# Optimization experiments

Hardware: AMD Instinct MI355X
Metric: run time of the kernel (lower is better)

## Reference

```python
import jax, jax.numpy as jnp
import numpy as np

SEQ, D = 4096, 1024  # vector_size == dimension == 1024


def setup_inputs() -> dict:
    key = jax.random.key(0)
    ks = jax.random.split(key, 7)
    s = 1.0 / np.sqrt(D)
    return {
        "X": jax.random.normal(ks[0], (SEQ, D), dtype=jnp.float32),
        "Wq": jax.random.normal(ks[1], (D, D), dtype=jnp.float32) * s,
        "bq": jax.random.normal(ks[2], (D,), dtype=jnp.float32) * s,
        "Wk": jax.random.normal(ks[3], (D, D), dtype=jnp.float32) * s,
        "bk": jax.random.normal(ks[4], (D,), dtype=jnp.float32) * s,
        "Wv": jax.random.normal(ks[5], (D, D), dtype=jnp.float32) * s,
        "bv": jax.random.normal(ks[6], (D,), dtype=jnp.float32) * s,
    }


def reference(X, Wq, bq, Wk, bk, Wv, bv):
    # Batched QKV projections (nn.Linear: x @ W^T + b), replacing the per-vector loop.
    Q = X @ Wq.T + bq            # [S, D]
    K = X @ Wk.T + bk            # [S, D]
    V = X @ Wv.T + bv            # [S, D]
    scale = 1.0 / jnp.sqrt(jnp.asarray(D, dtype=X.dtype))
    scores = (Q @ K.T) * scale   # [S, S]
    attn = jax.nn.softmax(scores, axis=1)
    return attn @ V              # [S, D]
```

## Files before the change

kernel.cpp:

```cpp
#include <hip/hip_runtime.h>
#include <hip/hip_bf16.h>
#include <stdint.h>


typedef __bf16 bf16_t;
typedef __bf16 bf16x4 __attribute__((ext_vector_type(4)));
typedef __bf16 bf16x8 __attribute__((ext_vector_type(8)));
typedef float f32x4 __attribute__((ext_vector_type(4)));

#define AS1 __attribute__((address_space(1)))
#define AS3 __attribute__((address_space(3)))

__device__ __forceinline__ void async_ld16(const void* g, void* l) {
  __builtin_amdgcn_global_load_lds((AS1 void*)g, (AS3 void*)l, 16, 0, 0);
}

template <int MODE>
__global__ __launch_bounds__(512, 2) void gemm8(
    const bf16_t* __restrict__ A, const bf16_t* __restrict__ B, const int ld,
    const int Klen, bf16_t* __restrict__ o0, bf16_t* __restrict__ o1,
    bf16_t* __restrict__ o2, const float* __restrict__ b0,
    const float* __restrict__ b1, const float* __restrict__ b2,
    float* __restrict__ fout, float* __restrict__ rowsum) {
  extern __shared__ bf16_t smem[];

  const int t = threadIdx.x;
  const int lane = t & 63;
  const int wave = t >> 6;
  const int wm = wave >> 2;
  const int wn = wave & 3;
  const int q = lane >> 4;
  const int l16 = lane & 15;
  const int xf = l16 & 7;

  int m0, n0, k0 = 0, zz = 0;
  const int bid = blockIdx.x;
  if constexpr (MODE == 0) {
    const int x = bid & 7, sl = bid >> 3;
    m0 = ((x >> 1) * 4 + (sl & 3)) * 256;
    n0 = ((x & 1) * 6 + (sl >> 2)) * 256;
  } else if constexpr (MODE == 1) {
    const int x = bid & 7, sl = bid >> 3;
    m0 = ((x >> 2) * 8 + (sl >> 2)) * 256;
    n0 = ((x & 3) * 4 + (sl & 3)) * 256;
  } else {
    const int x = bid & 7, sl = bid >> 3;
    zz = x >> 1;
    m0 = ((x & 1) * 8 + (sl >> 2)) * 256;
    n0 = (sl & 3) * 256;
    k0 = zz * Klen;
  }

  const int srow = t >> 3;
  const int c8s = ((t & 7) ^ (srow & 7)) * 8;
  const bf16_t* Ab = A + (size_t)(m0 + srow) * ld + k0 + c8s;
  const bf16_t* Bb = B + (size_t)(n0 + srow) * ld + k0 + c8s;
  const int tl8 = t * 8;

  const int aoff = (wm * 128 + l16) * 64;
  const int boff = (wn * 64 + l16) * 64;
  const int c0 = (q ^ xf) * 8;
  const int c1 = ((4 + q) ^ xf) * 8;

  f32x4 acc[8][4];
  const f32x4 zero4 = {0.f, 0.f, 0.f, 0.f};
#pragma unroll
  for (int i = 0; i < 8; ++i)
#pragma unroll
    for (int j = 0; j < 4; ++j) acc[i][j] = zero4;

  const int NT = Klen >> 6;
  bf16_t* buf0 = smem;
  bf16_t* buf1 = smem + 32768;

  auto STAGE = [&](int T, bf16_t* buf) {
    const size_t kk = (size_t)(T << 6);
    async_ld16(Ab + kk, buf + tl8);
    async_ld16(Ab + (size_t)64 * ld + kk, buf + 4096 + tl8);
    async_ld16(Ab + (size_t)128 * ld + kk, buf + 8192 + tl8);
    async_ld16(Ab + (size_t)192 * ld + kk, buf + 12288 + tl8);
    async_ld16(Bb + kk, buf + 16384 + tl8);
    async_ld16(Bb + (size_t)64 * ld + kk, buf + 16384 + 4096 + tl8);
    async_ld16(Bb + (size_t)128 * ld + kk, buf + 16384 + 8192 + tl8);
    async_ld16(Bb + (size_t)192 * ld + kk, buf + 16384 + 12288 + tl8);
  };

  STAGE(0, buf0);
  __syncthreads();

  for (int T = 0; T < NT; ++T) {
    bf16_t* cur = (T & 1) ? buf1 : buf0;
    bf16_t* nxt = (T & 1) ? buf0 : buf1;
    if (T + 1 < NT) STAGE(T + 1, nxt);

#pragma unroll
    for (int s = 0; s < 2; ++s) {
      const int cs = (s == 0) ? c0 : c1;
      bf16x8 fa[8], fb[4];
#pragma unroll
      for (int im = 0; im < 8; ++im)
        fa[im] = *(const bf16x8*)(cur + aoff + im * 1024 + cs);
#pragma unroll
      for (int j = 0; j < 4; ++j)
        fb[j] = *(const bf16x8*)(cur + 16384 + boff + j * 1024 + cs);
#pragma unroll
      for (int im = 0; im < 8; ++im)
#pragma unroll
        for (int j = 0; j < 4; ++j)
          acc[im][j] = __builtin_amdgcn_mfma_f32_16x16x32_bf16(
              fa[im], fb[j], acc[im][j], 0, 0, 0);
    }
    __syncthreads();
  }

  const int mW = m0 + wm * 128 + q * 4;

  if constexpr (MODE == 0) {
    const int sel = n0 >> 10;
    const int nl0 = (n0 & 1023) + wn * 64 + l16;
    if (sel < 2) {
      const float* bias = (sel == 0) ? b0 : b1;
      const float sc = (sel == 0) ? 0.03125f : 1.0f;
      bf16_t* dst = (sel == 0) ? o0 : o1;
      float bb[4];
#pragma unroll
      for (int j = 0; j < 4; ++j) bb[j] = bias[nl0 + j * 16];
#pragma unroll
      for (int im = 0; im < 8; ++im) {
        const int mr = mW + im * 16;
#pragma unroll
        for (int r = 0; r < 4; ++r)
#pragma unroll
          for (int j = 0; j < 4; ++j)
            dst[(size_t)(mr + r) * 1024 + nl0 + j * 16] =
                (bf16_t)((acc[im][j][r] + bb[j]) * sc);
      }
    } else {
      bf16_t* vs = smem;
      const int dg0 = n0 & 1023;
#pragma unroll
      for (int h = 0; h < 2; ++h) {
        if ((wn >> 1) == h) {
#pragma unroll
          for (int j = 0; j < 4; ++j) {
            const int dl = (wn & 1) * 64 + j * 16 + l16;
            const float bb = b2[dg0 + h * 128 + dl];
#pragma unroll
            for (int im = 0; im < 8; ++im) {
              bf16x4 v;
#pragma unroll
              for (int r = 0; r < 4; ++r) v[r] = (bf16_t)(acc[im][j][r] + bb);
              *(bf16x4*)(vs + dl * 264 + wm * 128 + im * 16 + q * 4) = v;
            }
          }
        }
        __syncthreads();
#pragma unroll
        for (int rr = 0; rr < 8; ++rr) {
          const int task = rr * 512 + t;
          const int row = task >> 5, ck = task & 31;
          *(bf16x8*)(o2 + (size_t)(dg0 + h * 128 + row) * 4096 + m0 + ck * 8) =
              *(const bf16x8*)(vs + row * 264 + ck * 8);
        }
        __syncthreads();
      }
    }
  } else if constexpr (MODE == 1) {
    float ps[8][4];
#pragma unroll
    for (int im = 0; im < 8; ++im)
#pragma unroll
      for (int r = 0; r < 4; ++r) ps[im][r] = 0.f;
    const int nb = n0 + wn * 64 + l16;
#pragma unroll
    for (int im = 0; im < 8; ++im) {
      const int mr = mW + im * 16;
#pragma unroll
      for (int r = 0; r < 4; ++r)
#pragma unroll
        for (int j = 0; j < 4; ++j) {
          const float e = __expf(acc[im][j][r]);
          ps[im][r] += e;
          o0[(size_t)(mr + r) * 4096 + nb + j * 16] = (bf16_t)e;
        }
    }
#pragma unroll
    for (int im = 0; im < 8; ++im)
#pragma unroll
      for (int r = 0; r < 4; ++r) {
        float v = ps[im][r];
        v += __shfl_xor(v, 1);
        v += __shfl_xor(v, 2);
        v += __shfl_xor(v, 4);
        v += __shfl_xor(v, 8);
        ps[im][r] = v;
      }
    if (l16 == 0) {
#pragma unroll
      for (int im = 0; im < 8; ++im)
#pragma unroll
        for (int r = 0; r < 4; ++r)
          atomicAdd(rowsum + mW + im * 16 + r, ps[im][r]);
    }
  } else {
    float inv[8][4];
#pragma unroll
    for (int im = 0; im < 8; ++im)
#pragma unroll
      for (int r = 0; r < 4; ++r)
        inv[im][r] = 1.0f / rowsum[mW + im * 16 + r];
    const int nb = n0 + wn * 64 + l16;
    if (zz < 3) {
      bf16_t* pp = (zz == 0) ? o0 : ((zz == 1) ? o1 : o2);
#pragma unroll
      for (int im = 0; im < 8; ++im) {
        const int mr = mW + im * 16;
#pragma unroll
        for (int r = 0; r < 4; ++r) {
          const float iv = inv[im][r];
#pragma unroll
          for (int j = 0; j < 4; ++j)
            pp[(size_t)(mr + r) * 1024 + nb + j * 16] =
                (bf16_t)(acc[im][j][r] * iv);
        }
      }
    } else {
#pragma unroll
      for (int im = 0; im < 8; ++im) {
        const int mr = mW + im * 16;
#pragma unroll
        for (int r = 0; r < 4; ++r) {
          const float iv = inv[im][r];
#pragma unroll
          for (int j = 0; j < 4; ++j)
            fout[(size_t)(mr + r) * 1024 + nb + j * 16] = acc[im][j][r] * iv;
        }
      }
    }
  }
}

__global__ __launch_bounds__(256) void cvt_all(
    const float* __restrict__ X, const float* __restrict__ Wq,
    const float* __restrict__ Wk, const float* __restrict__ Wv,
    bf16_t* __restrict__ Xb, bf16_t* __restrict__ Wb,
    float* __restrict__ rowsum) {
  int i = blockIdx.x * 256 + threadIdx.x;
  if (i >= 1835008) {
    rowsum[i - 1835008] = 0.f;
    return;
  }
  const float* src;
  bf16_t* dst;
  int off;
  if (i < 1048576) {
    src = X; dst = Xb; off = i;
  } else {
    const int w = i - 1048576;
    const int sel = w >> 18;
    off = w & 0x3FFFF;
    src = (sel == 0) ? Wq : ((sel == 1) ? Wk : Wv);
    dst = Wb + (size_t)sel * (1024 * 1024);
  }
  const float4 v = ((const float4*)src)[off];
  bf16x4 o;
  o[0] = (bf16_t)v.x; o[1] = (bf16_t)v.y; o[2] = (bf16_t)v.z; o[3] = (bf16_t)v.w;
  ((bf16x4*)dst)[off] = o;
}

__global__ __launch_bounds__(256) void reduce_out(
    const bf16_t* __restrict__ p0, const bf16_t* __restrict__ p1,
    const bf16_t* __restrict__ p2, float* __restrict__ out) {
  const int i = blockIdx.x * 256 + threadIdx.x;
  const bf16x8 a = ((const bf16x8*)p0)[i];
  const bf16x8 b = ((const bf16x8*)p1)[i];
  const bf16x8 c = ((const bf16x8*)p2)[i];
  float4 lo = ((const float4*)out)[2 * i];
  float4 hi = ((const float4*)out)[2 * i + 1];
  lo.x += (float)a[0] + (float)b[0] + (float)c[0];
  lo.y += (float)a[1] + (float)b[1] + (float)c[1];
  lo.z += (float)a[2] + (float)b[2] + (float)c[2];
  lo.w += (float)a[3] + (float)b[3] + (float)c[3];
  hi.x += (float)a[4] + (float)b[4] + (float)c[4];
  hi.y += (float)a[5] + (float)b[5] + (float)c[5];
  hi.z += (float)a[6] + (float)b[6] + (float)c[6];
  hi.w += (float)a[7] + (float)b[7] + (float)c[7];
  ((float4*)out)[2 * i] = lo;
  ((float4*)out)[2 * i + 1] = hi;
}

extern "C" void kernel_launch(void* const* d_in, const int* in_sizes, int n_in,
                              void* d_out, int out_size, void* d_ws,
                              size_t ws_size, hipStream_t stream) {
  const int S = 4096, D = 1024;
  const float* X  = (const float*)d_in[0];
  const float* Wq = (const float*)d_in[1];
  const float* bq = (const float*)d_in[2];
  const float* Wk = (const float*)d_in[3];
  const float* bk = (const float*)d_in[4];
  const float* Wv = (const float*)d_in[5];
  const float* bv = (const float*)d_in[6];
  float* out = (float*)d_out;

  bf16_t* Xb = (bf16_t*)d_ws;
  bf16_t* Wb = Xb + (size_t)S * D;
  bf16_t* Qb = Wb + (size_t)3 * D * D;
  bf16_t* Kb = Qb + (size_t)S * D;
  bf16_t* Vt = Kb + (size_t)S * D;
  bf16_t* Sc = Vt + (size_t)D * S;
  float* rowsum = (float*)(Sc + (size_t)S * S);

  static int attr_set = 0;
  if (!attr_set) {
    attr_set = 1;
    (void)hipFuncSetAttribute(reinterpret_cast<const void*>(gemm8<0>),
                              hipFuncAttributeMaxDynamicSharedMemorySize,
                              131072);
    (void)hipFuncSetAttribute(reinterpret_cast<const void*>(gemm8<1>),
                              hipFuncAttributeMaxDynamicSharedMemorySize,
                              131072);
    (void)hipFuncSetAttribute(reinterpret_cast<const void*>(gemm8<2>),
                              hipFuncAttributeMaxDynamicSharedMemorySize,
                              131072);
  }

  cvt_all<<<7184, 256, 0, stream>>>(X, Wq, Wk, Wv, Xb, Wb, rowsum);

  gemm8<0><<<192, 512, 131072, stream>>>(
      Xb, Wb, D, D, Qb, Kb, Vt, bq, bk, bv, nullptr, nullptr);
  gemm8<1><<<256, 512, 131072, stream>>>(
      Qb, Kb, D, D, Sc, nullptr, nullptr, nullptr, nullptr, nullptr, nullptr,
      rowsum);
  gemm8<2><<<256, 512, 131072, stream>>>(
      Sc, Vt, S, S / 4, Xb, Qb, Kb, nullptr, nullptr, nullptr, out, rowsum);
  reduce_out<<<S * D / 8 / 256, 256, 0, stream>>>(Xb, Qb, Kb, out);
}
```

Baseline: 205.0 us.

## Shrink GEMM tiles to 256x128 with single-buffered static LDS and higher occupancy

The three GEMM phases now use 256x128 output tiles computed by a 4x2 wave grid, with twice as many blocks. The double-buffered 128KB dynamic LDS is replaced by a single-buffered 48KB static buffer, and launch bounds ask for 4 blocks per CU. The goal is to hide memory latency through more resident blocks and a higher block count instead of software prefetch. The cost is that loads no longer overlap compute within a block. Each tile also does less MMA work per byte loaded, and the register budget becomes tighter.

Result: no change. 204.8 us, median of 2 (-0.1%).

```diff
diff --git a/kernel.cpp b/kernel.cpp
--- a/kernel.cpp
+++ b/kernel.cpp
@@ -16,19 +16,21 @@
 }
 
 template <int MODE>
-__global__ __launch_bounds__(512, 2) void gemm8(
+__global__ __launch_bounds__(512, 4) void gemm2(
     const bf16_t* __restrict__ A, const bf16_t* __restrict__ B, const int ld,
     const int Klen, bf16_t* __restrict__ o0, bf16_t* __restrict__ o1,
     bf16_t* __restrict__ o2, const float* __restrict__ b0,
     const float* __restrict__ b1, const float* __restrict__ b2,
     float* __restrict__ fout, float* __restrict__ rowsum) {
-  extern __shared__ bf16_t smem[];
+  __shared__ bf16_t smem[24576];
+  bf16_t* As = smem;
+  bf16_t* Bs = smem + 16384;
 
   const int t = threadIdx.x;
   const int lane = t & 63;
   const int wave = t >> 6;
-  const int wm = wave >> 2;
-  const int wn = wave & 3;
+  const int wm = wave >> 1;
+  const int wn = wave & 1;
   const int q = lane >> 4;
   const int l16 = lane & 15;
   const int xf = l16 & 7;
@@ -38,16 +40,16 @@
   if constexpr (MODE == 0) {
     const int x = bid & 7, sl = bid >> 3;
     m0 = ((x >> 1) * 4 + (sl & 3)) * 256;
-    n0 = ((x & 1) * 6 + (sl >> 2)) * 256;
+    n0 = ((x & 1) * 12 + (sl >> 2)) * 128;
   } else if constexpr (MODE == 1) {
     const int x = bid & 7, sl = bid >> 3;
-    m0 = ((x >> 2) * 8 + (sl >> 2)) * 256;
-    n0 = ((x & 3) * 4 + (sl & 3)) * 256;
+    m0 = ((x >> 2) * 8 + (sl >> 3)) * 256;
+    n0 = ((x & 3) * 8 + (sl & 7)) * 128;
   } else {
     const int x = bid & 7, sl = bid >> 3;
     zz = x >> 1;
-    m0 = ((x & 1) * 8 + (sl >> 2)) * 256;
-    n0 = (sl & 3) * 256;
+    m0 = ((x & 1) * 8 + (sl >> 3)) * 256;
+    n0 = (sl & 7) * 128;
     k0 = zz * Klen;
   }
 
@@ -57,54 +59,37 @@
   const bf16_t* Bb = B + (size_t)(n0 + srow) * ld + k0 + c8s;
   const int tl8 = t * 8;
 
-  const int aoff = (wm * 128 + l16) * 64;
-  const int boff = (wn * 64 + l16) * 64;
-  const int c0 = (q ^ xf) * 8;
-  const int c1 = ((4 + q) ^ xf) * 8;
-
-  f32x4 acc[8][4];
+  const int ar = wm * 64 + l16;
+  const int br = wn * 64 + l16;
+
+  f32x4 acc[4][4];
   const f32x4 zero4 = {0.f, 0.f, 0.f, 0.f};
 #pragma unroll
-  for (int i = 0; i < 8; ++i)
+  for (int i = 0; i < 4; ++i)
 #pragma unroll
     for (int j = 0; j < 4; ++j) acc[i][j] = zero4;
 
-  const int NT = Klen >> 6;
-  bf16_t* buf0 = smem;
-  bf16_t* buf1 = smem + 32768;
-
-  auto STAGE = [&](int T, bf16_t* buf) {
-    const size_t kk = (size_t)(T << 6);
-    async_ld16(Ab + kk, buf + tl8);
-    async_ld16(Ab + (size_t)64 * ld + kk, buf + 4096 + tl8);
-    async_ld16(Ab + (size_t)128 * ld + kk, buf + 8192 + tl8);
-    async_ld16(Ab + (size_t)192 * ld + kk, buf + 12288 + tl8);
-    async_ld16(Bb + kk, buf + 16384 + tl8);
-    async_ld16(Bb + (size_t)64 * ld + kk, buf + 16384 + 4096 + tl8);
-    async_ld16(Bb + (size_t)128 * ld + kk, buf + 16384 + 8192 + tl8);
-    async_ld16(Bb + (size_t)192 * ld + kk, buf + 16384 + 12288 + tl8);
-  };
-
-  STAGE(0, buf0);
-  __syncthreads();
-
-  for (int T = 0; T < NT; ++T) {
-    bf16_t* cur = (T & 1) ? buf1 : buf0;
-    bf16_t* nxt = (T & 1) ? buf0 : buf1;
-    if (T + 1 < NT) STAGE(T + 1, nxt);
+  for (int kt = 0; kt < Klen; kt += 64) {
+#pragma unroll
+    for (int rr = 0; rr < 4; ++rr)
+      async_ld16(Ab + kt + (size_t)(rr * 64) * ld, As + rr * 4096 + tl8);
+#pragma unroll
+    for (int rr = 0; rr < 2; ++rr)
+      async_ld16(Bb + kt + (size_t)(rr * 64) * ld, Bs + rr * 4096 + tl8);
+    __syncthreads();
 
 #pragma unroll
     for (int s = 0; s < 2; ++s) {
-      const int cs = (s == 0) ? c0 : c1;
-      bf16x8 fa[8], fb[4];
-#pragma unroll
-      for (int im = 0; im < 8; ++im)
-        fa[im] = *(const bf16x8*)(cur + aoff + im * 1024 + cs);
+      const int cs = ((s * 4 + q) ^ xf) * 8;
+      bf16x8 fa[4], fb[4];
+#pragma unroll
+      for (int im = 0; im < 4; ++im)
+        fa[im] = *(const bf16x8*)(As + (ar + im * 16) * 64 + cs);
 #pragma unroll
       for (int j = 0; j < 4; ++j)
-        fb[j] = *(const bf16x8*)(cur + 16384 + boff + j * 1024 + cs);
-#pragma unroll
-      for (int im = 0; im < 8; ++im)
+        fb[j] = *(const bf16x8*)(Bs + (br + j * 16) * 64 + cs);
+#pragma unroll
+      for (int im = 0; im < 4; ++im)
 #pragma unroll
         for (int j = 0; j < 4; ++j)
           acc[im][j] = __builtin_amdgcn_mfma_f32_16x16x32_bf16(
@@ -113,7 +98,7 @@
     __syncthreads();
   }
 
-  const int mW = m0 + wm * 128 + q * 4;
+  const int mBase = m0 + wm * 64 + q * 4;
 
   if constexpr (MODE == 0) {
     const int sel = n0 >> 10;
@@ -126,8 +111,8 @@
 #pragma unroll
       for (int j = 0; j < 4; ++j) bb[j] = bias[nl0 + j * 16];
 #pragma unroll
-      for (int im = 0; im < 8; ++im) {
-        const int mr = mW + im * 16;
+      for (int im = 0; im < 4; ++im) {
+        const int mr = mBase + im * 16;
 #pragma unroll
         for (int r = 0; r < 4; ++r)
 #pragma unroll
@@ -140,41 +125,41 @@
       const int dg0 = n0 & 1023;
 #pragma unroll
       for (int h = 0; h < 2; ++h) {
-        if ((wn >> 1) == h) {
+        if (wn == h) {
 #pragma unroll
           for (int j = 0; j < 4; ++j) {
-            const int dl = (wn & 1) * 64 + j * 16 + l16;
-            const float bb = b2[dg0 + h * 128 + dl];
-#pragma unroll
-            for (int im = 0; im < 8; ++im) {
+            const int dl = j * 16 + l16;
+            const float bb = b2[dg0 + h * 64 + dl];
+#pragma unroll
+            for (int im = 0; im < 4; ++im) {
               bf16x4 v;
 #pragma unroll
               for (int r = 0; r < 4; ++r) v[r] = (bf16_t)(acc[im][j][r] + bb);
-              *(bf16x4*)(vs + dl * 264 + wm * 128 + im * 16 + q * 4) = v;
+              *(bf16x4*)(vs + dl * 264 + wm * 64 + im * 16 + q * 4) = v;
             }
           }
         }
         __syncthreads();
 #pragma unroll
-        for (int rr = 0; rr < 8; ++rr) {
+        for (int rr = 0; rr < 4; ++rr) {
           const int task = rr * 512 + t;
           const int row = task >> 5, ck = task & 31;
-          *(bf16x8*)(o2 + (size_t)(dg0 + h * 128 + row) * 4096 + m0 + ck * 8) =
+          *(bf16x8*)(o2 + (size_t)(dg0 + h * 64 + row) * 4096 + m0 + ck * 8) =
               *(const bf16x8*)(vs + row * 264 + ck * 8);
         }
         __syncthreads();
       }
     }
   } else if constexpr (MODE == 1) {
-    float ps[8][4];
-#pragma unroll
-    for (int im = 0; im < 8; ++im)
+    float ps[4][4];
+#pragma unroll
+    for (int im = 0; im < 4; ++im)
 #pragma unroll
       for (int r = 0; r < 4; ++r) ps[im][r] = 0.f;
     const int nb = n0 + wn * 64 + l16;
 #pragma unroll
-    for (int im = 0; im < 8; ++im) {
-      const int mr = mW + im * 16;
+    for (int im = 0; im < 4; ++im) {
+      const int mr = mBase + im * 16;
 #pragma unroll
       for (int r = 0; r < 4; ++r)
 #pragma unroll
@@ -185,7 +170,7 @@
         }
     }
 #pragma unroll
-    for (int im = 0; im < 8; ++im)
+    for (int im = 0; im < 4; ++im)
 #pragma unroll
       for (int r = 0; r < 4; ++r) {
         float v = ps[im][r];
@@ -197,24 +182,24 @@
       }
     if (l16 == 0) {
 #pragma unroll
-      for (int im = 0; im < 8; ++im)
+      for (int im = 0; im < 4; ++im)
 #pragma unroll
         for (int r = 0; r < 4; ++r)
-          atomicAdd(rowsum + mW + im * 16 + r, ps[im][r]);
+          atomicAdd(rowsum + mBase + im * 16 + r, ps[im][r]);
     }
   } else {
-    float inv[8][4];
-#pragma unroll
-    for (int im = 0; im < 8; ++im)
+    float inv[4][4];
+#pragma unroll
+    for (int im = 0; im < 4; ++im)
 #pragma unroll
       for (int r = 0; r < 4; ++r)
-        inv[im][r] = 1.0f / rowsum[mW + im * 16 + r];
+        inv[im][r] = 1.0f / rowsum[mBase + im * 16 + r];
     const int nb = n0 + wn * 64 + l16;
     if (zz < 3) {
       bf16_t* pp = (zz == 0) ? o0 : ((zz == 1) ? o1 : o2);
 #pragma unroll
-      for (int im = 0; im < 8; ++im) {
-        const int mr = mW + im * 16;
+      for (int im = 0; im < 4; ++im) {
+        const int mr = mBase + im * 16;
 #pragma unroll
         for (int r = 0; r < 4; ++r) {
           const float iv = inv[im][r];
@@ -226,8 +211,8 @@
       }
     } else {
 #pragma unroll
-      for (int im = 0; im < 8; ++im) {
-        const int mr = mW + im * 16;
+      for (int im = 0; im < 4; ++im) {
+        const int mr = mBase + im * 16;
 #pragma unroll
         for (int r = 0; r < 4; ++r) {
           const float iv = inv[im][r];
@@ -310,28 +295,14 @@
   bf16_t* Sc = Vt + (size_t)D * S;
   float* rowsum = (float*)(Sc + (size_t)S * S);
 
-  static int attr_set = 0;
-  if (!attr_set) {
-    attr_set = 1;
-    (void)hipFuncSetAttribute(reinterpret_cast<const void*>(gemm8<0>),
-                              hipFuncAttributeMaxDynamicSharedMemorySize,
-                              131072);
-    (void)hipFuncSetAttribute(reinterpret_cast<const void*>(gemm8<1>),
-                              hipFuncAttributeMaxDynamicSharedMemorySize,
-                              131072);
-    (void)hipFuncSetAttribute(reinterpret_cast<const void*>(gemm8<2>),
-                              hipFuncAttributeMaxDynamicSharedMemorySize,
-                              131072);
-  }
-
   cvt_all<<<7184, 256, 0, stream>>>(X, Wq, Wk, Wv, Xb, Wb, rowsum);
 
-  gemm8<0><<<192, 512, 131072, stream>>>(
+  gemm2<0><<<384, 512, 0, stream>>>(
       Xb, Wb, D, D, Qb, Kb, Vt, bq, bk, bv, nullptr, nullptr);
-  gemm8<1><<<256, 512, 131072, stream>>>(
+  gemm2<1><<<512, 512, 0, stream>>>(
       Qb, Kb, D, D, Sc, nullptr, nullptr, nullptr, nullptr, nullptr, nullptr,
       rowsum);
-  gemm8<2><<<256, 512, 131072, stream>>>(
+  gemm2<2><<<512, 512, 0, stream>>>(
       Sc, Vt, S, S / 4, Xb, Qb, Kb, nullptr, nullptr, nullptr, out, rowsum);
   reduce_out<<<S * D / 8 / 256, 256, 0, stream>>>(Xb, Qb, Kb, out);
 }
```

## Rewrite GEMM main loop as ping-pong pipeline with fine-grained async staging

Applied to the files above, without the earlier changes.

Replaces the simple double-buffered K loop with a manually scheduled pipeline. Each 64-wide K tile is split into two 32-wide halves with a new 4-chunk XOR swizzle. Global-to-LDS loads for upcoming tiles are interleaved between MFMA groups, guarded by explicit vmcnt/lgkmcnt waits and raw barriers, and the MFMA sections are raised with s_setprio. The goal is to hide global load latency and overlap LDS reads with matrix math. The cost is many more barriers per tile and fragile hand-placed wait counts, which risk stalls or races.

After: 216.2 us. +5.5%, slower.

```diff
diff --git a/kernel.cpp b/kernel.cpp
--- a/kernel.cpp
+++ b/kernel.cpp
@@ -15,8 +15,13 @@
   __builtin_amdgcn_global_load_lds((AS1 void*)g, (AS3 void*)l, 16, 0, 0);
 }
 
+#define BAR() __builtin_amdgcn_s_barrier()
+#define LGKM0() asm volatile("s_waitcnt lgkmcnt(0)" ::: "memory")
+#define VM6() asm volatile("s_waitcnt vmcnt(6)" ::: "memory")
+#define VM0() asm volatile("s_waitcnt vmcnt(0)" ::: "memory")
+
 template <int MODE>
-__global__ __launch_bounds__(512, 2) void gemm8(
+__global__ __launch_bounds__(512, 2) void gemm8p(
     const bf16_t* __restrict__ A, const bf16_t* __restrict__ B, const int ld,
     const int Klen, bf16_t* __restrict__ o0, bf16_t* __restrict__ o1,
     bf16_t* __restrict__ o2, const float* __restrict__ b0,
@@ -31,7 +36,6 @@
   const int wn = wave & 3;
   const int q = lane >> 4;
   const int l16 = lane & 15;
-  const int xf = l16 & 7;
 
   int m0, n0, k0 = 0, zz = 0;
   const int bid = blockIdx.x;
@@ -51,16 +55,21 @@
     k0 = zz * Klen;
   }
 
-  const int srow = t >> 3;
-  const int c8s = ((t & 7) ^ (srow & 7)) * 8;
-  const bf16_t* Ab = A + (size_t)(m0 + srow) * ld + k0 + c8s;
-  const bf16_t* Bb = B + (size_t)(n0 + srow) * ld + k0 + c8s;
+  const int srow2 = t >> 2;
+  const int c4s = (((t & 3) ^ (srow2 & 3)) * 8);
+  const bf16_t* Ab = A + (size_t)(m0 + srow2) * ld + k0 + c4s;
+  const bf16_t* Bb = B + (size_t)(n0 + srow2) * ld + k0 + c4s;
   const int tl8 = t * 8;
-
-  const int aoff = (wm * 128 + l16) * 64;
-  const int boff = (wn * 64 + l16) * 64;
-  const int c0 = (q ^ xf) * 8;
-  const int c1 = ((4 + q) ^ xf) * 8;
+  const size_t r128 = (size_t)128 * ld;
+
+  bf16_t* A0 = smem;
+  bf16_t* B0 = smem + 16384;
+  bf16_t* A1 = smem + 32768;
+  bf16_t* B1s = smem + 49152;
+
+  const int xsl = (q ^ (l16 & 3)) * 8;
+  const int aBase = (wm * 128 + l16) * 32 + xsl;
+  const int bBase = (wn * 64 + l16) * 32 + xsl;
 
   f32x4 acc[8][4];
   const f32x4 zero4 = {0.f, 0.f, 0.f, 0.f};
@@ -70,47 +79,68 @@
     for (int j = 0; j < 4; ++j) acc[i][j] = zero4;
 
   const int NT = Klen >> 6;
-  bf16_t* buf0 = smem;
-  bf16_t* buf1 = smem + 32768;
-
-  auto STAGE = [&](int T, bf16_t* buf) {
-    const size_t kk = (size_t)(T << 6);
-    async_ld16(Ab + kk, buf + tl8);
-    async_ld16(Ab + (size_t)64 * ld + kk, buf + 4096 + tl8);
-    async_ld16(Ab + (size_t)128 * ld + kk, buf + 8192 + tl8);
-    async_ld16(Ab + (size_t)192 * ld + kk, buf + 12288 + tl8);
-    async_ld16(Bb + kk, buf + 16384 + tl8);
-    async_ld16(Bb + (size_t)64 * ld + kk, buf + 16384 + 4096 + tl8);
-    async_ld16(Bb + (size_t)128 * ld + kk, buf + 16384 + 8192 + tl8);
-    async_ld16(Bb + (size_t)192 * ld + kk, buf + 16384 + 12288 + tl8);
+
+  auto STG = [&](const bf16_t* gb, bf16_t* lbuf, int tile, int ksh) {
+    const int ko = tile * 64 + ksh * 32;
+    async_ld16(gb + ko, lbuf + ksh * 8192 + tl8);
+    async_ld16(gb + r128 + ko, lbuf + ksh * 8192 + 4096 + tl8);
   };
 
-  STAGE(0, buf0);
-  __syncthreads();
-
-  for (int T = 0; T < NT; ++T) {
-    bf16_t* cur = (T & 1) ? buf1 : buf0;
-    bf16_t* nxt = (T & 1) ? buf0 : buf1;
-    if (T + 1 < NT) STAGE(T + 1, nxt);
-
-#pragma unroll
-    for (int s = 0; s < 2; ++s) {
-      const int cs = (s == 0) ? c0 : c1;
-      bf16x8 fa[8], fb[4];
-#pragma unroll
-      for (int im = 0; im < 8; ++im)
-        fa[im] = *(const bf16x8*)(cur + aoff + im * 1024 + cs);
-#pragma unroll
-      for (int j = 0; j < 4; ++j)
-        fb[j] = *(const bf16x8*)(cur + 16384 + boff + j * 1024 + cs);
-#pragma unroll
-      for (int im = 0; im < 8; ++im)
-#pragma unroll
-        for (int j = 0; j < 4; ++j)
-          acc[im][j] = __builtin_amdgcn_mfma_f32_16x16x32_bf16(
-              fa[im], fb[j], acc[im][j], 0, 0, 0);
-    }
-    __syncthreads();
+  STG(Bb, B0, 0, 0); STG(Ab, A0, 0, 0); STG(Bb, B0, 0, 1); STG(Ab, A0, 0, 1);
+  STG(Bb, B1s, 1, 0); STG(Ab, A1, 1, 0); STG(Bb, B1s, 1, 1);
+  VM6();
+  BAR();
+
+  for (int it = 0; it < NT / 2; ++it) {
+    const int T1 = 2 * it + 1, T2 = 2 * it + 2, T3 = 2 * it + 3;
+    const bool s2 = T2 < NT, s3 = T3 < NT;
+    bf16x8 fa[4], fb0[4], fb1[4];
+
+#define RDA(bufA, ks, img)                                              \
+  _Pragma("unroll") for (int im = 0; im < 4; ++im) fa[im] =             \
+      *(const bf16x8*)(bufA + (ks) * 8192 + aBase + ((img) * 4 + im) * 512);
+#define RDB(bufB, ks, fb)                                               \
+  _Pragma("unroll") for (int j = 0; j < 4; ++j) fb[j] =                 \
+      *(const bf16x8*)(bufB + (ks) * 8192 + bBase + j * 512);
+#define MM(fb, img)                                                     \
+  __builtin_amdgcn_s_setprio(1);                                        \
+  _Pragma("unroll") for (int im = 0; im < 4; ++im)                      \
+      _Pragma("unroll") for (int j = 0; j < 4; ++j)                     \
+          acc[(img) * 4 + im][j] = __builtin_amdgcn_mfma_f32_16x16x32_bf16( \
+              fa[im], fb[j], acc[(img) * 4 + im][j], 0, 0, 0);          \
+  __builtin_amdgcn_s_setprio(0);
+
+    RDA(A0, 0, 0); RDB(B0, 0, fb0);
+    STG(Ab, A1, T1, 1);
+    BAR(); LGKM0(); MM(fb0, 0); BAR();
+    RDA(A0, 0, 1);
+    if (s2) STG(Bb, B0, T2, 0);
+    BAR(); LGKM0(); MM(fb0, 1); BAR();
+    RDA(A0, 1, 0); RDB(B0, 1, fb1);
+    if (s2) STG(Ab, A0, T2, 0);
+    BAR(); LGKM0(); MM(fb1, 0); BAR();
+    RDA(A0, 1, 1);
+    if (s2) STG(Bb, B0, T2, 1);
+    BAR(); LGKM0(); MM(fb1, 1);
+    if (s2) { VM6(); } else { VM0(); }
+    BAR();
+    RDA(A1, 0, 0); RDB(B1s, 0, fb0);
+    if (s2) STG(Ab, A0, T2, 1);
+    BAR(); LGKM0(); MM(fb0, 0); BAR();
+    RDA(A1, 0, 1);
+    if (s3) STG(Bb, B1s, T3, 0);
+    BAR(); LGKM0(); MM(fb0, 1); BAR();
+    RDA(A1, 1, 0); RDB(B1s, 1, fb1);
+    if (s3) STG(Ab, A1, T3, 0);
+    BAR(); LGKM0(); MM(fb1, 0); BAR();
+    RDA(A1, 1, 1);
+    if (s3) STG(Bb, B1s, T3, 1);
+    BAR(); LGKM0(); MM(fb1, 1);
+    if (s3) { VM6(); } else { VM0(); }
+    BAR();
+#undef RDA
+#undef RDB
+#undef MM
   }
 
   const int mW = m0 + wm * 128 + q * 4;
@@ -313,25 +343,25 @@
   static int attr_set = 0;
   if (!attr_set) {
     attr_set = 1;
-    (void)hipFuncSetAttribute(reinterpret_cast<const void*>(gemm8<0>),
+    (void)hipFuncSetAttribute(reinterpret_cast<const void*>(gemm8p<0>),
                               hipFuncAttributeMaxDynamicSharedMemorySize,
                               131072);
-    (void)hipFuncSetAttribute(reinterpret_cast<const void*>(gemm8<1>),
+    (void)hipFuncSetAttribute(reinterpret_cast<const void*>(gemm8p<1>),
                               hipFuncAttributeMaxDynamicSharedMemorySize,
                               131072);
-    (void)hipFuncSetAttribute(reinterpret_cast<const void*>(gemm8<2>),
+    (void)hipFuncSetAttribute(reinterpret_cast<const void*>(gemm8p<2>),
                               hipFuncAttributeMaxDynamicSharedMemorySize,
                               131072);
   }
 
   cvt_all<<<7184, 256, 0, stream>>>(X, Wq, Wk, Wv, Xb, Wb, rowsum);
 
-  gemm8<0><<<192, 512, 131072, stream>>>(
+  gemm8p<0><<<192, 512, 131072, stream>>>(
       Xb, Wb, D, D, Qb, Kb, Vt, bq, bk, bv, nullptr, nullptr);
-  gemm8<1><<<256, 512, 131072, stream>>>(
+  gemm8p<1><<<256, 512, 131072, stream>>>(
       Qb, Kb, D, D, Sc, nullptr, nullptr, nullptr, nullptr, nullptr, nullptr,
       rowsum);
-  gemm8<2><<<256, 512, 131072, stream>>>(
+  gemm8p<2><<<256, 512, 131072, stream>>>(
       Sc, Vt, S, S / 4, Xb, Qb, Kb, nullptr, nullptr, nullptr, out, rowsum);
   reduce_out<<<S * D / 8 / 256, 256, 0, stream>>>(Xb, Qb, Kb, out);
 }
```

## Interleave split async loads with MFMA phases using fine-grained waitcnt barriers

Applied to the files above, without the earlier changes.

Replaces the two-buffer stage-then-compute loop with an 8-phase unrolled schedule. The schedule issues half-tile global-to-LDS loads between quarter-tile MFMA blocks, uses explicit vmcnt/lgkmcnt waits and raw s_barrier instead of __syncthreads, and raises wave priority around MFMA bursts. The aim is to hide global load latency and barrier stalls behind matrix math in all three GEMMs. It adds a lot of barriers and hand-placed waitcnts, which can cause subtle races, and the loop assumes NT is even.

New measurement: 284.7 us. 1.39x slower.

```diff
diff --git a/kernel.cpp b/kernel.cpp
--- a/kernel.cpp
+++ b/kernel.cpp
@@ -15,8 +15,13 @@
   __builtin_amdgcn_global_load_lds((AS1 void*)g, (AS3 void*)l, 16, 0, 0);
 }
 
+#define BAR() __builtin_amdgcn_s_barrier()
+#define LGKM0() asm volatile("s_waitcnt lgkmcnt(0)" ::: "memory")
+#define VM4() asm volatile("s_waitcnt vmcnt(4)" ::: "memory")
+#define VM0() asm volatile("s_waitcnt vmcnt(0)" ::: "memory")
+
 template <int MODE>
-__global__ __launch_bounds__(512, 2) void gemm8(
+__global__ __launch_bounds__(512, 2) void gemm8q(
     const bf16_t* __restrict__ A, const bf16_t* __restrict__ B, const int ld,
     const int Klen, bf16_t* __restrict__ o0, bf16_t* __restrict__ o1,
     bf16_t* __restrict__ o2, const float* __restrict__ b0,
@@ -57,6 +62,11 @@
   const bf16_t* Bb = B + (size_t)(n0 + srow) * ld + k0 + c8s;
   const int tl8 = t * 8;
 
+  bf16_t* A0 = smem;
+  bf16_t* B0 = smem + 16384;
+  bf16_t* A1 = smem + 32768;
+  bf16_t* B1s = smem + 49152;
+
   const int aoff = (wm * 128 + l16) * 64;
   const int boff = (wn * 64 + l16) * 64;
   const int c0 = (q ^ xf) * 8;
@@ -70,47 +80,105 @@
     for (int j = 0; j < 4; ++j) acc[i][j] = zero4;
 
   const int NT = Klen >> 6;
-  bf16_t* buf0 = smem;
-  bf16_t* buf1 = smem + 32768;
-
-  auto STAGE = [&](int T, bf16_t* buf) {
-    const size_t kk = (size_t)(T << 6);
-    async_ld16(Ab + kk, buf + tl8);
-    async_ld16(Ab + (size_t)64 * ld + kk, buf + 4096 + tl8);
-    async_ld16(Ab + (size_t)128 * ld + kk, buf + 8192 + tl8);
-    async_ld16(Ab + (size_t)192 * ld + kk, buf + 12288 + tl8);
-    async_ld16(Bb + kk, buf + 16384 + tl8);
-    async_ld16(Bb + (size_t)64 * ld + kk, buf + 16384 + 4096 + tl8);
-    async_ld16(Bb + (size_t)128 * ld + kk, buf + 16384 + 8192 + tl8);
-    async_ld16(Bb + (size_t)192 * ld + kk, buf + 16384 + 12288 + tl8);
+
+  auto STG = [&](const bf16_t* gb, bf16_t* lbuf, int tile, int h) {
+    const int ko = tile << 6;
+    async_ld16(gb + (size_t)(h * 128) * ld + ko, lbuf + h * 8192 + tl8);
+    async_ld16(gb + (size_t)(h * 128 + 64) * ld + ko,
+               lbuf + h * 8192 + 4096 + tl8);
   };
 
-  STAGE(0, buf0);
-  __syncthreads();
-
-  for (int T = 0; T < NT; ++T) {
-    bf16_t* cur = (T & 1) ? buf1 : buf0;
-    bf16_t* nxt = (T & 1) ? buf0 : buf1;
-    if (T + 1 < NT) STAGE(T + 1, nxt);
-
-#pragma unroll
-    for (int s = 0; s < 2; ++s) {
-      const int cs = (s == 0) ? c0 : c1;
-      bf16x8 fa[8], fb[4];
-#pragma unroll
-      for (int im = 0; im < 8; ++im)
-        fa[im] = *(const bf16x8*)(cur + aoff + im * 1024 + cs);
-#pragma unroll
-      for (int j = 0; j < 4; ++j)
-        fb[j] = *(const bf16x8*)(cur + 16384 + boff + j * 1024 + cs);
-#pragma unroll
-      for (int im = 0; im < 8; ++im)
-#pragma unroll
-        for (int j = 0; j < 4; ++j)
-          acc[im][j] = __builtin_amdgcn_mfma_f32_16x16x32_bf16(
-              fa[im], fb[j], acc[im][j], 0, 0, 0);
-    }
-    __syncthreads();
+  STG(Ab, A0, 0, 0); STG(Ab, A0, 0, 1);
+  STG(Bb, B0, 0, 0); STG(Bb, B0, 0, 1);
+  STG(Ab, A1, 1, 0); STG(Ab, A1, 1, 1);
+  VM4();
+  BAR();
+
+  for (int it = 0; it < NT / 2; ++it) {
+    const int Tp1 = 2 * it + 1, Tp2 = 2 * it + 2, Tp3 = 2 * it + 3;
+    const bool s2 = Tp2 < NT, s3 = Tp3 < NT;
+    bf16x8 faA[4][2], faB[4][2], fb[4][2];
+
+#define MM(fa_, ks_, base_)                                                  \
+  __builtin_amdgcn_s_setprio(1);                                             \
+  _Pragma("unroll") for (int im = 0; im < 4; ++im)                           \
+      _Pragma("unroll") for (int j = 0; j < 4; ++j)                          \
+          acc[(base_) + im][j] = __builtin_amdgcn_mfma_f32_16x16x32_bf16(    \
+              fa_[im][ks_], fb[j][ks_], acc[(base_) + im][j], 0, 0, 0);      \
+  __builtin_amdgcn_s_setprio(0);
+
+#pragma unroll
+    for (int im = 0; im < 4; ++im) {
+      faA[im][0] = *(const bf16x8*)(A0 + aoff + im * 1024 + c0);
+      faA[im][1] = *(const bf16x8*)(A0 + aoff + im * 1024 + c1);
+    }
+#pragma unroll
+    for (int j = 0; j < 4; ++j)
+      fb[j][0] = *(const bf16x8*)(B0 + boff + j * 1024 + c0);
+    STG(Bb, B1s, Tp1, 0);
+    BAR(); LGKM0();
+    MM(faA, 0, 0);
+    BAR();
+
+#pragma unroll
+    for (int im = 0; im < 4; ++im) {
+      faB[im][0] = *(const bf16x8*)(A0 + aoff + (im + 4) * 1024 + c0);
+      faB[im][1] = *(const bf16x8*)(A0 + aoff + (im + 4) * 1024 + c1);
+    }
+    STG(Bb, B1s, Tp1, 1);
+    BAR(); LGKM0();
+    MM(faB, 0, 4);
+    BAR();
+
+#pragma unroll
+    for (int j = 0; j < 4; ++j)
+      fb[j][1] = *(const bf16x8*)(B0 + boff + j * 1024 + c1);
+    if (s2) STG(Ab, A0, Tp2, 0);
+    BAR(); LGKM0();
+    MM(faA, 1, 0);
+    BAR();
+
+    if (s2) STG(Ab, A0, Tp2, 1);
+    MM(faB, 1, 4);
+    if (s2) { VM4(); } else { VM0(); }
+    BAR();
+
+#pragma unroll
+    for (int im = 0; im < 4; ++im) {
+      faA[im][0] = *(const bf16x8*)(A1 + aoff + im * 1024 + c0);
+      faA[im][1] = *(const bf16x8*)(A1 + aoff + im * 1024 + c1);
+    }
+#pragma unroll
+    for (int j = 0; j < 4; ++j)
+      fb[j][0] = *(const bf16x8*)(B1s + boff + j * 1024 + c0);
+    if (s2) STG(Bb, B0, Tp2, 0);
+    BAR(); LGKM0();
+    MM(faA, 0, 0);
+    BAR();
+
+#pragma unroll
+    for (int im = 0; im < 4; ++im) {
+      faB[im][0] = *(const bf16x8*)(A1 + aoff + (im + 4) * 1024 + c0);
+      faB[im][1] = *(const bf16x8*)(A1 + aoff + (im + 4) * 1024 + c1);
+    }
+    if (s2) STG(Bb, B0, Tp2, 1);
+    BAR(); LGKM0();
+    MM(faB, 0, 4);
+    BAR();
+
+#pragma unroll
+    for (int j = 0; j < 4; ++j)
+      fb[j][1] = *(const bf16x8*)(B1s + boff + j * 1024 + c1);
+    if (s3) STG(Ab, A1, Tp3, 0);
+    BAR(); LGKM0();
+    MM(faA, 1, 0);
+    BAR();
+
+    if (s3) STG(Ab, A1, Tp3, 1);
+    MM(faB, 1, 4);
+    if (s3) { VM4(); } else { VM0(); }
+    BAR();
+#undef MM
   }
 
   const int mW = m0 + wm * 128 + q * 4;
@@ -313,25 +381,25 @@
   static int attr_set = 0;
   if (!attr_set) {
     attr_set = 1;
-    (void)hipFuncSetAttribute(reinterpret_cast<const void*>(gemm8<0>),
+    (void)hipFuncSetAttribute(reinterpret_cast<const void*>(gemm8q<0>),
                               hipFuncAttributeMaxDynamicSharedMemorySize,
                               131072);
-    (void)hipFuncSetAttribute(reinterpret_cast<const void*>(gemm8<1>),
+    (void)hipFuncSetAttribute(reinterpret_cast<const void*>(gemm8q<1>),
                               hipFuncAttributeMaxDynamicSharedMemorySize,
                               131072);
-    (void)hipFuncSetAttribute(reinterpret_cast<const void*>(gemm8<2>),
+    (void)hipFuncSetAttribute(reinterpret_cast<const void*>(gemm8q<2>),
                               hipFuncAttributeMaxDynamicSharedMemorySize,
                               131072);
   }
 
   cvt_all<<<7184, 256, 0, stream>>>(X, Wq, Wk, Wv, Xb, Wb, rowsum);
 
-  gemm8<0><<<192, 512, 131072, stream>>>(
+  gemm8q<0><<<192, 512, 131072, stream>>>(
       Xb, Wb, D, D, Qb, Kb, Vt, bq, bk, bv, nullptr, nullptr);
-  gemm8<1><<<256, 512, 131072, stream>>>(
+  gemm8q<1><<<256, 512, 131072, stream>>>(
       Qb, Kb, D, D, Sc, nullptr, nullptr, nullptr, nullptr, nullptr, nullptr,
       rowsum);
-  gemm8<2><<<256, 512, 131072, stream>>>(
+  gemm8q<2><<<256, 512, 131072, stream>>>(
       Sc, Vt, S, S / 4, Xb, Qb, Kb, nullptr, nullptr, nullptr, out, rowsum);
   reduce_out<<<S * D / 8 / 256, 256, 0, stream>>>(Xb, Qb, Kb, out);
 }
```
